# Kernel tuning notes

Measured on AMD Instinct MI355X. Metric: run time of the kernel, lower is better.

The kernel has to match this reference:

```python
import jax, jax.numpy as jnp
import numpy as np

# ---- model / data constants ----
B, N, D, L = 32, 96, 64, 5          # graphs, nodes per graph, hidden, layers
EP = 768                             # directed edges per graph (symmetrized in to_dense)
NODE_VOCAB = 11                      # matches LocalFWL2(..., 11, 5, 'instance')
EDGE_VOCAB = 5                       # edge labels 0..4; index 5 = 'no edge' embedding row
EPS = 1e-5


def setup_inputs() -> dict:
    key = jax.random.key(0)
    ks = jax.random.split(key, 12)
    # block-contiguous batch: graph b owns nodes [b*N, (b+1)*N)
    x = jax.random.randint(ks[0], (B * N,), 0, NODE_VOCAB)
    u = jax.random.randint(ks[1], (B, EP), 0, N)
    v = jax.random.randint(ks[2], (B, EP), 0, N)
    off = (jnp.arange(B) * N)[:, None]
    edge_index = jnp.stack([(u + off).reshape(-1), (v + off).reshape(-1)], axis=0)
    edge_attr = jax.random.randint(ks[3], (B * EP,), 0, EDGE_VOCAB)
    s = 0.1
    inv = 1.0 / np.sqrt(D)
    return {
        "x": x,
        "edge_index": edge_index,
        "edge_attr": edge_attr,
        "node_emb": jax.random.normal(ks[4], (NODE_VOCAB, D), jnp.float32) * s,
        "edge_emb": jax.random.normal(ks[5], (EDGE_VOCAB + 1, D), jnp.float32) * s,
        "W1": jax.random.normal(ks[6], (L, D, D), jnp.float32) * inv,
        "b1": jnp.zeros((L, D), jnp.float32),
        "W2": jax.random.normal(ks[7], (L, D, D), jnp.float32) * inv,
        "b2": jnp.zeros((L, D), jnp.float32),
        "Wm": jax.random.normal(ks[8], (L, D, D), jnp.float32) * inv,
        "bm": jnp.zeros((L, D), jnp.float32),
        "gamma": jnp.ones((L, D), jnp.float32),
        "beta": jnp.zeros((L, D), jnp.float32),
        "pool_w": jax.random.normal(ks[9], (D, 1), jnp.float32) * inv,
        "pool_b": jnp.zeros((1,), jnp.float32),
    }


def reference(x, edge_index, edge_attr, node_emb, edge_emb,
              W1, b1, W2, b2, Wm, bm, gamma, beta, pool_w, pool_b):
    # ---- to_dense: sparse edge list -> dense per-graph edge-label matrix ----
    g = edge_index[0] // N
    u = edge_index[0] % N
    v = edge_index[1] % N
    A = jnp.full((B, N, N), EDGE_VOCAB, dtype=jnp.int32)        # EDGE_VOCAB = no-edge
    ea = edge_attr.astype(jnp.int32)
    A = A.at[g, u, v].set(ea)
    A = A.at[g, v, u].set(ea)                                    # undirected
    adj = (A != EDGE_VOCAB).astype(node_emb.dtype)               # [B,N,N]

    # ---- pair-state init: W_uv = h_u + h_v + edge_emb(A_uv) ----
    H = node_emb[x.reshape(B, N)]                                # [B,N,D]
    W = H[:, :, None, :] + H[:, None, :, :] + edge_emb[A]        # [B,N,N,D]

    # ---- local FWL(2) layers ----
    for l in range(L):
        h1 = jax.nn.relu(jnp.einsum('buwd,de->buwe', W, W1[l]) + b1[l])
        h2 = jax.nn.relu(jnp.einsum('bwvd,de->bwve', W, W2[l]) + b2[l])
        # aggregate over w restricted to neighbors of v (local FWL2)
        M = jnp.einsum('buwd,bwv,bwvd->buvd', h1, adj, h2)       # [B,N,N,D]
        W = W + jnp.einsum('buvd,de->buve', M, Wm[l]) + bm[l]
        # instance norm over the pair dims (u,v), per graph, per channel
        mu = W.mean(axis=(1, 2), keepdims=True)
        var = W.var(axis=(1, 2), keepdims=True)
        W = gamma[l] * (W - mu) * jax.lax.rsqrt(var + EPS) + beta[l]
        W = jax.nn.relu(W)

    # ---- pooling: sum over all pairs, then Linear(D, 1), squeeze ----
    pooled = W.sum(axis=(1, 2))                                  # [B,D]
    return (pooled @ pool_w + pool_b).squeeze(-1)                # [B]
```

## Files before the change

kernel.cpp:

```cpp
#include <hip/hip_runtime.h>
#include <hip/hip_bf16.h>

#define B_ 32
#define N_ 96
#define D_ 64
#define L_ 5
#define BE_ 24576
#define NN_ 9216
#define BNN_ 294912
#define EPS_ 1e-5f
#define INV_NN (1.0f/9216.0f)

typedef unsigned short u16;
typedef unsigned int u32;
typedef __attribute__((ext_vector_type(8))) short bf16x8;
typedef __attribute__((ext_vector_type(4))) float f32x4;

__device__ __forceinline__ float bf2f(u16 r){ return __uint_as_float(((u32)r) << 16); }
__device__ __forceinline__ u32 f2bf(float f){
  u32 u = __float_as_uint(f);
  return (u + 0x7fffu + ((u >> 16) & 1u)) >> 16;
}
__device__ __forceinline__ u32 pack2(float lo, float hi){
  return f2bf(lo) | (f2bf(hi) << 16);
}

__global__ void k_scatter(const int* __restrict__ ei, const int* __restrict__ ea,
                          int* __restrict__ A)
{
  int e = blockIdx.x * 256 + threadIdx.x;
  if (e >= BE_) return;
  int a = ei[e], bnode = ei[BE_ + e];
  int g = a / N_;
  int u = a % N_;
  int v = bnode % N_;
  int lab = ea[e] & 7;
  int base = g * NN_;
  atomicMax(&A[base + u * N_ + v], ((e + 1) << 3) | lab);
  atomicMax(&A[base + v * N_ + u], ((BE_ + e + 1) << 3) | lab);
}

__launch_bounds__(256)
__global__ void k_winit(const int* __restrict__ x, const int* __restrict__ A,
                        const float* __restrict__ nemb, const float* __restrict__ eemb,
                        u16* __restrict__ W)
{
  int gid = blockIdx.x * 256 + threadIdx.x;
  int d = (gid & 15) * 4;
  int p = gid >> 4;
  int b = p / NN_;
  int rem = p % NN_;
  int u = rem / N_;
  int v = rem % N_;
  int xu = x[b * N_ + u], xv = x[b * N_ + v];
  int pk = A[p];
  int lab = pk ? (pk & 7) : 5;
  float4 nu = *(const float4*)(nemb + xu * 64 + d);
  float4 nv = *(const float4*)(nemb + xv * 64 + d);
  float4 ee = *(const float4*)(eemb + lab * 64 + d);
  uint2 o;
  o.x = pack2(nu.x + nv.x + ee.x, nu.y + nv.y + ee.y);
  o.y = pack2(nu.z + nv.z + ee.z, nu.w + nv.w + ee.w);
  ((uint2*)W)[gid] = o;
}

__global__ void k_prep(const float* __restrict__ W1, const float* __restrict__ W2,
                       const float* __restrict__ Wm, u16* __restrict__ WT)
{
  int idx = blockIdx.x * 256 + threadIdx.x;
  if (idx >= 15 * 4096) return;
  int l3 = idx >> 12;
  int r  = idx & 4095;
  int e = r >> 6, d = r & 63;
  int l = l3 / 3, which = l3 % 3;
  const float* s = which == 0 ? W1 : which == 1 ? W2 : Wm;
  WT[idx] = (u16)f2bf(s[l * 4096 + d * 64 + e]);
}

__launch_bounds__(128)
__global__ void k_ns(const float* __restrict__ pst, const float* __restrict__ gml,
                     const float* __restrict__ btl, float* __restrict__ nsF)
{
  __shared__ float nsS[128];
  const int b = blockIdx.x;
  const int tid = threadIdx.x;
  const float* p = pst + ((size_t)b * 144) * 128 + tid;
  float a0 = 0.f, a1 = 0.f, a2 = 0.f, a3 = 0.f;
  for (int i = 0; i < 144; i += 4) {
    a0 += p[(size_t)i * 128];
    a1 += p[(size_t)(i + 1) * 128];
    a2 += p[(size_t)(i + 2) * 128];
    a3 += p[(size_t)(i + 3) * 128];
  }
  nsS[tid] = (a0 + a1) + (a2 + a3);
  __syncthreads();
  if (tid < 64) {
    float S1 = nsS[tid], S2 = nsS[64 + tid];
    float mu = S1 * INV_NN;
    float var = fmaf(S2, INV_NN, -mu * mu);
    float s0 = gml[tid] * rsqrtf(var + EPS_);
    nsF[((size_t)b * 64 + tid) * 2]     = s0;
    nsF[((size_t)b * 64 + tid) * 2 + 1] = fmaf(-mu, s0, btl[tid]);
  }
}

__launch_bounds__(256, 8)
__global__ void k_lin2(const u16* __restrict__ W, const u16* __restrict__ WT1,
                       const u16* __restrict__ WT2,
                       const float* __restrict__ b1l, const float* __restrict__ b2l,
                       const int* __restrict__ A, const float* __restrict__ nsF,
                       int use_norm, u16* __restrict__ h1, u16* __restrict__ g2)
{
  __shared__ u16 Cs[64 * 136];
  const int tid = threadIdx.x;
  const int wave = tid >> 6, lane = tid & 63;
  const int lm = lane & 15, lg = lane >> 4;
  const int b = blockIdx.x / 72;
  const int qbase = (blockIdx.x % 72) * 128;

  float sc[2][8], sh[2][8];
  if (use_norm) {
    #pragma unroll
    for (int s = 0; s < 2; ++s) {
      int d0 = s * 32 + lg * 8;
      #pragma unroll
      for (int j = 0; j < 8; j += 2) {
        float4 t = *(const float4*)(nsF + ((size_t)b * 64 + d0 + j) * 2);
        sc[s][j] = t.x; sh[s][j] = t.y; sc[s][j + 1] = t.z; sh[s][j + 1] = t.w;
      }
    }
  } else {
    #pragma unroll
    for (int s = 0; s < 2; ++s)
      #pragma unroll
      for (int j = 0; j < 8; ++j) { sc[s][j] = 1.f; sh[s][j] = 0.f; }
  }

  bf16x8 bF[2][2];
  int flags[2];
  #pragma unroll
  for (int qt = 0; qt < 2; ++qt) {
    int q = qbase + wave * 32 + qt * 16 + lm;
    const u16* wrow = W + ((size_t)b * NN_ + q) * 64;
    flags[qt] = A[b * NN_ + q];
    #pragma unroll
    for (int s = 0; s < 2; ++s) {
      bf16x8 raw = *(const bf16x8*)(wrow + s * 32 + lg * 8);
      if (use_norm) {
        bf16x8 bb;
        #pragma unroll
        for (int j = 0; j < 8; ++j) {
          float v = bf2f((u16)raw[j]);
          v = fmaxf(fmaf(v, sc[s][j], sh[s][j]), 0.f);
          bb[j] = (short)f2bf(v);
        }
        bF[qt][s] = bb;
      } else {
        bF[qt][s] = raw;
      }
    }
  }

  const f32x4 zf = {0.f, 0.f, 0.f, 0.f};

  {
    bf16x8 aF[4][2];
    #pragma unroll
    for (int et = 0; et < 4; ++et)
      #pragma unroll
      for (int s = 0; s < 2; ++s)
        aF[et][s] = *(const bf16x8*)(WT1 + (et * 16 + lm) * 64 + s * 32 + lg * 8);
    float4 bsv[4];
    #pragma unroll
    for (int et = 0; et < 4; ++et) bsv[et] = *(const float4*)(b1l + et * 16 + lg * 4);
    #pragma unroll
    for (int qt = 0; qt < 2; ++qt) {
      f32x4 acc[4] = {zf, zf, zf, zf};
      #pragma unroll
      for (int s = 0; s < 2; ++s)
        #pragma unroll
        for (int et = 0; et < 4; ++et)
          acc[et] = __builtin_amdgcn_mfma_f32_16x16x32_bf16(aF[et][s], bF[qt][s], acc[et], 0, 0, 0);
      int col = wave * 32 + qt * 16 + lm;
      #pragma unroll
      for (int et = 0; et < 4; ++et) {
        float bv[4] = {bsv[et].x, bsv[et].y, bsv[et].z, bsv[et].w};
        #pragma unroll
        for (int r = 0; r < 4; ++r)
          Cs[(et * 16 + lg * 4 + r) * 136 + col] = (u16)f2bf(fmaxf(acc[et][r] + bv[r], 0.f));
      }
    }
  }
  __syncthreads();
  {
    u16* ob = h1 + (size_t)b * 64 * NN_ + qbase;
    for (int i = tid; i < 1024; i += 256) {
      int e = i >> 4, qc = (i & 15) * 8;
      uint4 val = *(const uint4*)&Cs[e * 136 + qc];
      *(uint4*)(ob + (size_t)e * NN_ + qc) = val;
    }
  }
  __syncthreads();

  {
    bf16x8 aF[4][2];
    #pragma unroll
    for (int et = 0; et < 4; ++et)
      #pragma unroll
      for (int s = 0; s < 2; ++s)
        aF[et][s] = *(const bf16x8*)(WT2 + (et * 16 + lm) * 64 + s * 32 + lg * 8);
    float4 bsv[4];
    #pragma unroll
    for (int et = 0; et < 4; ++et) bsv[et] = *(const float4*)(b2l + et * 16 + lg * 4);
    #pragma unroll
    for (int qt = 0; qt < 2; ++qt) {
      f32x4 acc[4] = {zf, zf, zf, zf};
      #pragma unroll
      for (int s = 0; s < 2; ++s)
        #pragma unroll
        for (int et = 0; et < 4; ++et)
          acc[et] = __builtin_amdgcn_mfma_f32_16x16x32_bf16(aF[et][s], bF[qt][s], acc[et], 0, 0, 0);
      int col = wave * 32 + qt * 16 + lm;
      #pragma unroll
      for (int et = 0; et < 4; ++et) {
        float bv[4] = {bsv[et].x, bsv[et].y, bsv[et].z, bsv[et].w};
        #pragma unroll
        for (int r = 0; r < 4; ++r) {
          float v = fmaxf(acc[et][r] + bv[r], 0.f);
          if (!flags[qt]) v = 0.f;
          Cs[(et * 16 + lg * 4 + r) * 136 + col] = (u16)f2bf(v);
        }
      }
    }
  }
  __syncthreads();
  {
    u16* ob = g2 + (size_t)b * 64 * NN_ + qbase;
    for (int i = tid; i < 1024; i += 256) {
      int e = i >> 4, qc = (i & 15) * 8;
      uint4 val = *(const uint4*)&Cs[e * 136 + qc];
      *(uint4*)(ob + (size_t)e * NN_ + qc) = val;
    }
  }
}

__launch_bounds__(256, 4)
__global__ void k_einsum(const u16* __restrict__ h1, const u16* __restrict__ g2n,
                         u16* __restrict__ M)
{
  __shared__ u32 Bt[96 * 60];
  u16* Cst = (u16*)Bt;
  const int tid = threadIdx.x;
  const int wave = tid >> 6, lane = tid & 63;
  const int lm = lane & 15, lg = lane >> 4;
  const int bd = blockIdx.x;
  const u16* h1p = h1 + (size_t)bd * NN_;
  const u16* g2p = g2n + (size_t)bd * NN_;
  const int u0 = (wave & 1) * 48, v0 = (wave >> 1) * 48;

  #pragma unroll
  for (int it = 0; it < 9; ++it) {
    int p = it * 256 + tid;
    int wp = p / 48, vh = (p % 48) * 2;
    u32 a = *(const u32*)(g2p + (2 * wp) * 96 + vh);
    u32 c = *(const u32*)(g2p + (2 * wp + 1) * 96 + vh);
    Bt[vh * 60 + wp]       = (a & 0xffffu) | (c << 16);
    Bt[(vh + 1) * 60 + wp] = (a >> 16) | (c & 0xffff0000u);
  }

  bf16x8 aF[3][3];
  #pragma unroll
  for (int t = 0; t < 3; ++t)
    #pragma unroll
    for (int s = 0; s < 3; ++s)
      aF[t][s] = *(const bf16x8*)(h1p + (u0 + t * 16 + lm) * 96 + s * 32 + lg * 8);
  __syncthreads();

  const f32x4 zf = {0.f, 0.f, 0.f, 0.f};
  f32x4 acc[3][3];
  #pragma unroll
  for (int i = 0; i < 3; ++i)
    #pragma unroll
    for (int j = 0; j < 3; ++j) acc[i][j] = zf;

  #pragma unroll
  for (int s = 0; s < 3; ++s) {
    bf16x8 bb[3];
    #pragma unroll
    for (int vt = 0; vt < 3; ++vt)
      bb[vt] = *(const bf16x8*)&Bt[(v0 + vt * 16 + lm) * 60 + s * 16 + lg * 4];
    #pragma unroll
    for (int ut = 0; ut < 3; ++ut)
      #pragma unroll
      for (int vt = 0; vt < 3; ++vt)
        acc[ut][vt] = __builtin_amdgcn_mfma_f32_16x16x32_bf16(aF[ut][s], bb[vt], acc[ut][vt], 0, 0, 0);
  }
  __syncthreads();

  #pragma unroll
  for (int ut = 0; ut < 3; ++ut)
    #pragma unroll
    for (int vt = 0; vt < 3; ++vt)
      #pragma unroll
      for (int r = 0; r < 4; ++r)
        Cst[(u0 + ut * 16 + lg * 4 + r) * 104 + v0 + vt * 16 + lm] = (u16)f2bf(acc[ut][vt][r]);
  __syncthreads();
  u16* Mp = M + (size_t)bd * NN_;
  for (int i = tid; i < 1152; i += 256) {
    int u = i / 12, vc = (i % 12) * 8;
    uint4 val = *(const uint4*)&Cst[u * 104 + vc];
    *(uint4*)(Mp + u * 96 + vc) = val;
  }
}

__launch_bounds__(128)
__global__ void k_update(const u16* __restrict__ M, const u16* __restrict__ WmT,
                         const float* __restrict__ bml, u16* __restrict__ W,
                         const float* __restrict__ nsF, int use_norm,
                         float* __restrict__ pst)
{
  __shared__ u16 Mt[64 * 64];
  __shared__ float red[2][128];
  const int tid = threadIdx.x;
  const int wave = tid >> 6, lane = tid & 63;
  const int lm = lane & 15, lg = lane >> 4;
  const int b = blockIdx.x / 144;
  const int qi = blockIdx.x % 144;
  const int qblk = qi * 64;

  bf16x8 aF[4][2];
  #pragma unroll
  for (int et = 0; et < 4; ++et)
    #pragma unroll
    for (int s = 0; s < 2; ++s)
      aF[et][s] = *(const bf16x8*)(WmT + (et * 16 + lm) * 64 + s * 32 + lg * 8);

  uint2 wres[2][4];
  #pragma unroll
  for (int qtL = 0; qtL < 2; ++qtL) {
    int qg = qblk + (wave * 2 + qtL) * 16 + lm;
    const u16* Wp = W + ((size_t)b * NN_ + qg) * 64;
    #pragma unroll
    for (int et = 0; et < 4; ++et)
      wres[qtL][et] = *(const uint2*)(Wp + et * 16 + lg * 4);
  }

  float scn[4][4], shn[4][4];
  if (use_norm) {
    #pragma unroll
    for (int et = 0; et < 4; ++et) {
      int e0 = et * 16 + lg * 4;
      float4 t0 = *(const float4*)(nsF + ((size_t)b * 64 + e0) * 2);
      float4 t1 = *(const float4*)(nsF + ((size_t)b * 64 + e0) * 2 + 4);
      scn[et][0] = t0.x; shn[et][0] = t0.y; scn[et][1] = t0.z; shn[et][1] = t0.w;
      scn[et][2] = t1.x; shn[et][2] = t1.y; scn[et][3] = t1.z; shn[et][3] = t1.w;
    }
  } else {
    #pragma unroll
    for (int et = 0; et < 4; ++et)
      #pragma unroll
      for (int r = 0; r < 4; ++r) { scn[et][r] = 1.f; shn[et][r] = 0.f; }
  }

  {
    const int dpl = tid >> 1;
    const int qob = tid & 1;
    const u16* Mb = M + (size_t)(b * 64 + dpl) * NN_ + qblk;
    #pragma unroll
    for (int t = 0; t < 4; ++t) {
      int qo = qob + t * 2;
      uint4 v = *(const uint4*)(Mb + qo * 8);
      u32 ws[4] = {v.x, v.y, v.z, v.w};
      #pragma unroll
      for (int h = 0; h < 4; ++h) {
        int j0 = h * 2;
        int q0 = qo * 8 + j0;
        int slot0 = (dpl >> 3) ^ j0 ^ (qo & 7);
        int slot1 = (dpl >> 3) ^ (j0 + 1) ^ (qo & 7);
        Mt[q0 * 64 + slot0 * 8 + (dpl & 7)]       = (u16)(ws[h] & 0xffffu);
        Mt[(q0 + 1) * 64 + slot1 * 8 + (dpl & 7)] = (u16)(ws[h] >> 16);
      }
    }
  }
  __syncthreads();

  const f32x4 zf = {0.f, 0.f, 0.f, 0.f};
  f32x4 acc[2][4];
  #pragma unroll
  for (int i = 0; i < 2; ++i)
    #pragma unroll
    for (int j = 0; j < 4; ++j) acc[i][j] = zf;

  #pragma unroll
  for (int qtL = 0; qtL < 2; ++qtL) {
    int ql = (wave * 2 + qtL) * 16 + lm;
    bf16x8 bF[2];
    #pragma unroll
    for (int s = 0; s < 2; ++s) {
      int slot = (s * 4 + lg) ^ (ql & 7) ^ ((ql >> 3) & 7);
      bF[s] = *(const bf16x8*)&Mt[ql * 64 + slot * 8];
    }
    #pragma unroll
    for (int s = 0; s < 2; ++s)
      #pragma unroll
      for (int et = 0; et < 4; ++et)
        acc[qtL][et] = __builtin_amdgcn_mfma_f32_16x16x32_bf16(aF[et][s], bF[s], acc[qtL][et], 0, 0, 0);
  }

  float s1[4][4], s2[4][4];
  #pragma unroll
  for (int i = 0; i < 4; ++i)
    #pragma unroll
    for (int j = 0; j < 4; ++j) { s1[i][j] = 0.f; s2[i][j] = 0.f; }

  #pragma unroll
  for (int et = 0; et < 4; ++et) {
    int e0 = et * 16 + lg * 4;
    float4 bs = *(const float4*)(bml + e0);
    float bv[4] = {bs.x, bs.y, bs.z, bs.w};
    #pragma unroll
    for (int qtL = 0; qtL < 2; ++qtL) {
      int qg = qblk + (wave * 2 + qtL) * 16 + lm;
      u16* Wp = W + ((size_t)b * NN_ + qg) * 64 + e0;
      uint2 wo = wres[qtL][et];
      float wv[4] = {bf2f((u16)(wo.x & 0xffff)), bf2f((u16)(wo.x >> 16)),
                     bf2f((u16)(wo.y & 0xffff)), bf2f((u16)(wo.y >> 16))};
      float o[4];
      #pragma unroll
      for (int r = 0; r < 4; ++r) {
        float res = use_norm ? fmaxf(fmaf(wv[r], scn[et][r], shn[et][r]), 0.f) : wv[r];
        float val = acc[qtL][et][r] + bv[r] + res;
        o[r] = val;
        s1[et][r] += val;
        s2[et][r] = fmaf(val, val, s2[et][r]);
      }
      uint2 ov;
      ov.x = pack2(o[0], o[1]);
      ov.y = pack2(o[2], o[3]);
      *(uint2*)Wp = ov;
    }
  }

  #pragma unroll
  for (int et = 0; et < 4; ++et)
    #pragma unroll
    for (int r = 0; r < 4; ++r) {
      float a = s1[et][r], c = s2[et][r];
      a += __shfl_xor(a, 1, 64); a += __shfl_xor(a, 2, 64);
      a += __shfl_xor(a, 4, 64); a += __shfl_xor(a, 8, 64);
      c += __shfl_xor(c, 1, 64); c += __shfl_xor(c, 2, 64);
      c += __shfl_xor(c, 4, 64); c += __shfl_xor(c, 8, 64);
      if (lm == 0) {
        int e = et * 16 + lg * 4 + r;
        red[wave][e]      = a;
        red[wave][64 + e] = c;
      }
    }
  __syncthreads();
  if (tid < 128)
    pst[((size_t)b * 144 + qi) * 128 + tid] = red[0][tid] + red[1][tid];
}

__launch_bounds__(256)
__global__ void k_pool(const u16* __restrict__ W,
                       const float* __restrict__ nsF,
                       const float* __restrict__ pw, const float* __restrict__ pb,
                       float* __restrict__ out)
{
  const int b = blockIdx.x / 24;
  const int chunk = blockIdx.x % 24;
  const int tid = threadIdx.x;
  const int e = tid & 63;
  float scl = nsF[((size_t)b * 64 + e) * 2];
  float shf = nsF[((size_t)b * 64 + e) * 2 + 1];
  float pwv = pw[e];
  const u16* base = W + (size_t)b * NN_ * 64 + chunk * 24576;
  float s = 0.f;
  for (int k = 0; k < 96; k++) {
    float w = bf2f(base[k * 256 + tid]);
    s += fmaxf(fmaf(w, scl, shf), 0.f) * pwv;
  }
  for (int o = 32; o; o >>= 1) s += __shfl_down(s, o, 64);
  __shared__ float rs[4];
  if ((tid & 63) == 0) rs[tid >> 6] = s;
  __syncthreads();
  if (tid == 0) {
    float t = rs[0] + rs[1] + rs[2] + rs[3];
    if (chunk == 0) t += pb[0];
    atomicAdd(&out[b], t);
  }
}

extern "C" void kernel_launch(void* const* d_in, const int* in_sizes, int n_in,
                              void* d_out, int out_size, void* d_ws, size_t ws_size,
                              hipStream_t stream) {
  const int*   x    = (const int*)d_in[0];
  const int*   ei   = (const int*)d_in[1];
  const int*   ea   = (const int*)d_in[2];
  const float* nemb = (const float*)d_in[3];
  const float* eemb = (const float*)d_in[4];
  const float* W1   = (const float*)d_in[5];
  const float* b1   = (const float*)d_in[6];
  const float* W2   = (const float*)d_in[7];
  const float* b2   = (const float*)d_in[8];
  const float* Wm   = (const float*)d_in[9];
  const float* bm   = (const float*)d_in[10];
  const float* gm   = (const float*)d_in[11];
  const float* bt   = (const float*)d_in[12];
  const float* pw   = (const float*)d_in[13];
  const float* pb   = (const float*)d_in[14];

  char* ws = (char*)d_ws;
  const size_t OFF_A  = 0;
  const size_t OFF_W  = 1179648;
  const size_t OFF_H1 = 38928384;
  const size_t OFF_G2 = 76677120;
  const size_t OFF_M  = 114425856;
  const size_t OFF_PS = 152174592;
  const size_t OFF_NF = 154533888;
  const size_t OFF_WT = 154550272;
  const size_t NEED   = OFF_WT + 122880;
  if (ws_size < NEED) return;

  int*   A     = (int*)(ws + OFF_A);
  u16*   W     = (u16*)(ws + OFF_W);
  u16*   h1    = (u16*)(ws + OFF_H1);
  u16*   g2n   = (u16*)(ws + OFF_G2);
  u16*   M     = (u16*)(ws + OFF_M);
  float* pst   = (float*)(ws + OFF_PS);
  float* nsF   = (float*)(ws + OFF_NF);
  u16*   WT    = (u16*)(ws + OFF_WT);
  float* out   = (float*)d_out;

  hipMemsetAsync(A, 0, 1179648, stream);
  hipMemsetAsync(out, 0, 32 * sizeof(float), stream);

  k_prep<<<240, 256, 0, stream>>>(W1, W2, Wm, WT);
  k_scatter<<<96, 256, 0, stream>>>(ei, ea, A);
  k_winit<<<18432, 256, 0, stream>>>(x, A, nemb, eemb, W);

  for (int l = 0; l < L_; l++) {
    int un = (l > 0);
    if (un)
      k_ns<<<32, 128, 0, stream>>>(pst, gm + (l - 1) * 64, bt + (l - 1) * 64, nsF);
    k_lin2<<<2304, 256, 0, stream>>>(W, WT + (l * 3 + 0) * 4096, WT + (l * 3 + 1) * 4096,
                                     b1 + l * 64, b2 + l * 64, A, nsF, un, h1, g2n);
    k_einsum<<<2048, 256, 0, stream>>>(h1, g2n, M);
    k_update<<<4608, 128, 0, stream>>>(M, WT + (l * 3 + 2) * 4096, bm + l * 64, W,
                                       nsF, un, pst);
  }
  k_ns<<<32, 128, 0, stream>>>(pst, gm + 4 * 64, bt + 4 * 64, nsF);
  k_pool<<<768, 256, 0, stream>>>(W, nsF, pw, pb, out);
}
```

Measured before the change: 633.4 us.

## Fuse instance-norm stats finalize into consumers via atomic per-graph sums

Removes the separate k_ns kernel launches by having k_update atomically accumulate per-graph channel sums and sums of squares into a per-layer stats buffer. Consumer kernels (k_lin2, k_update, k_pool) then compute mean, variance, scale and shift on the fly from those sums. This saves five small launches and their serialization gaps. In exchange it adds float atomics, which make the sums nondeterministic, plus redundant rsqrt work in every block. It also drops the occupancy hint on k_lin2.

Result: no change. 621.7 us (-1.8%).

```diff
diff --git a/kernel.cpp b/kernel.cpp
--- a/kernel.cpp
+++ b/kernel.cpp
@@ -77,56 +77,42 @@
   WT[idx] = (u16)f2bf(s[l * 4096 + d * 64 + e]);
 }
 
-__launch_bounds__(128)
-__global__ void k_ns(const float* __restrict__ pst, const float* __restrict__ gml,
-                     const float* __restrict__ btl, float* __restrict__ nsF)
-{
-  __shared__ float nsS[128];
-  const int b = blockIdx.x;
-  const int tid = threadIdx.x;
-  const float* p = pst + ((size_t)b * 144) * 128 + tid;
-  float a0 = 0.f, a1 = 0.f, a2 = 0.f, a3 = 0.f;
-  for (int i = 0; i < 144; i += 4) {
-    a0 += p[(size_t)i * 128];
-    a1 += p[(size_t)(i + 1) * 128];
-    a2 += p[(size_t)(i + 2) * 128];
-    a3 += p[(size_t)(i + 3) * 128];
-  }
-  nsS[tid] = (a0 + a1) + (a2 + a3);
-  __syncthreads();
-  if (tid < 64) {
-    float S1 = nsS[tid], S2 = nsS[64 + tid];
-    float mu = S1 * INV_NN;
-    float var = fmaf(S2, INV_NN, -mu * mu);
-    float s0 = gml[tid] * rsqrtf(var + EPS_);
-    nsF[((size_t)b * 64 + tid) * 2]     = s0;
-    nsF[((size_t)b * 64 + tid) * 2 + 1] = fmaf(-mu, s0, btl[tid]);
-  }
-}
-
-__launch_bounds__(256, 8)
+__launch_bounds__(256)
 __global__ void k_lin2(const u16* __restrict__ W, const u16* __restrict__ WT1,
                        const u16* __restrict__ WT2,
                        const float* __restrict__ b1l, const float* __restrict__ b2l,
-                       const int* __restrict__ A, const float* __restrict__ nsF,
+                       const int* __restrict__ A,
+                       const float* __restrict__ stp, const float* __restrict__ gml,
+                       const float* __restrict__ btl,
                        int use_norm, u16* __restrict__ h1, u16* __restrict__ g2)
 {
   __shared__ u16 Cs[64 * 136];
+  __shared__ float nsS[128];
   const int tid = threadIdx.x;
   const int wave = tid >> 6, lane = tid & 63;
   const int lm = lane & 15, lg = lane >> 4;
   const int b = blockIdx.x / 72;
   const int qbase = (blockIdx.x % 72) * 128;
 
+  if (use_norm) {
+    if (tid < 128) nsS[tid] = stp[(size_t)b * 128 + tid];
+    __syncthreads();
+  }
+
   float sc[2][8], sh[2][8];
   if (use_norm) {
     #pragma unroll
     for (int s = 0; s < 2; ++s) {
       int d0 = s * 32 + lg * 8;
       #pragma unroll
-      for (int j = 0; j < 8; j += 2) {
-        float4 t = *(const float4*)(nsF + ((size_t)b * 64 + d0 + j) * 2);
-        sc[s][j] = t.x; sh[s][j] = t.y; sc[s][j + 1] = t.z; sh[s][j + 1] = t.w;
+      for (int j = 0; j < 8; ++j) {
+        int d = d0 + j;
+        float S1 = nsS[d], S2 = nsS[64 + d];
+        float mu = S1 * INV_NN;
+        float var = fmaf(S2, INV_NN, -mu * mu);
+        float s0 = gml[d] * rsqrtf(var + EPS_);
+        sc[s][j] = s0;
+        sh[s][j] = fmaf(-mu, s0, btl[d]);
       }
     }
   } else {
@@ -316,11 +302,13 @@
 __launch_bounds__(128)
 __global__ void k_update(const u16* __restrict__ M, const u16* __restrict__ WmT,
                          const float* __restrict__ bml, u16* __restrict__ W,
-                         const float* __restrict__ nsF, int use_norm,
-                         float* __restrict__ pst)
+                         const float* __restrict__ stp, const float* __restrict__ gml,
+                         const float* __restrict__ btl, int use_norm,
+                         float* __restrict__ sto)
 {
   __shared__ u16 Mt[64 * 64];
   __shared__ float red[2][128];
+  __shared__ float nsS[128];
   const int tid = threadIdx.x;
   const int wave = tid >> 6, lane = tid & 63;
   const int lm = lane & 15, lg = lane >> 4;
@@ -328,6 +316,10 @@
   const int qi = blockIdx.x % 144;
   const int qblk = qi * 64;
 
+  if (use_norm) {
+    if (tid < 128) nsS[tid] = stp[(size_t)b * 128 + tid];
+  }
+
   bf16x8 aF[4][2];
   #pragma unroll
   for (int et = 0; et < 4; ++et)
@@ -343,23 +335,6 @@
     #pragma unroll
     for (int et = 0; et < 4; ++et)
       wres[qtL][et] = *(const uint2*)(Wp + et * 16 + lg * 4);
-  }
-
-  float scn[4][4], shn[4][4];
-  if (use_norm) {
-    #pragma unroll
-    for (int et = 0; et < 4; ++et) {
-      int e0 = et * 16 + lg * 4;
-      float4 t0 = *(const float4*)(nsF + ((size_t)b * 64 + e0) * 2);
-      float4 t1 = *(const float4*)(nsF + ((size_t)b * 64 + e0) * 2 + 4);
-      scn[et][0] = t0.x; shn[et][0] = t0.y; scn[et][1] = t0.z; shn[et][1] = t0.w;
-      scn[et][2] = t1.x; shn[et][2] = t1.y; scn[et][3] = t1.z; shn[et][3] = t1.w;
-    }
-  } else {
-    #pragma unroll
-    for (int et = 0; et < 4; ++et)
-      #pragma unroll
-      for (int r = 0; r < 4; ++r) { scn[et][r] = 1.f; shn[et][r] = 0.f; }
   }
 
   {
@@ -383,6 +358,29 @@
     }
   }
   __syncthreads();
+
+  float scn[4][4], shn[4][4];
+  if (use_norm) {
+    #pragma unroll
+    for (int et = 0; et < 4; ++et) {
+      int e0 = et * 16 + lg * 4;
+      #pragma unroll
+      for (int r = 0; r < 4; ++r) {
+        int e = e0 + r;
+        float S1 = nsS[e], S2 = nsS[64 + e];
+        float mu = S1 * INV_NN;
+        float var = fmaf(S2, INV_NN, -mu * mu);
+        float s0 = gml[e] * rsqrtf(var + EPS_);
+        scn[et][r] = s0;
+        shn[et][r] = fmaf(-mu, s0, btl[e]);
+      }
+    }
+  } else {
+    #pragma unroll
+    for (int et = 0; et < 4; ++et)
+      #pragma unroll
+      for (int r = 0; r < 4; ++r) { scn[et][r] = 1.f; shn[et][r] = 0.f; }
+  }
 
   const f32x4 zf = {0.f, 0.f, 0.f, 0.f};
   f32x4 acc[2][4];
@@ -458,21 +456,29 @@
     }
   __syncthreads();
   if (tid < 128)
-    pst[((size_t)b * 144 + qi) * 128 + tid] = red[0][tid] + red[1][tid];
+    atomicAdd(&sto[(size_t)b * 128 + tid], red[0][tid] + red[1][tid]);
 }
 
 __launch_bounds__(256)
 __global__ void k_pool(const u16* __restrict__ W,
-                       const float* __restrict__ nsF,
+                       const float* __restrict__ stp,
+                       const float* __restrict__ gml, const float* __restrict__ btl,
                        const float* __restrict__ pw, const float* __restrict__ pb,
                        float* __restrict__ out)
 {
+  __shared__ float nsS[128];
   const int b = blockIdx.x / 24;
   const int chunk = blockIdx.x % 24;
   const int tid = threadIdx.x;
+  if (tid < 128) nsS[tid] = stp[(size_t)b * 128 + tid];
+  __syncthreads();
   const int e = tid & 63;
-  float scl = nsF[((size_t)b * 64 + e) * 2];
-  float shf = nsF[((size_t)b * 64 + e) * 2 + 1];
+  float S1 = nsS[e], S2 = nsS[64 + e];
+  float mu = S1 * INV_NN;
+  float var = fmaf(S2, INV_NN, -mu * mu);
+  float rsig = rsqrtf(var + EPS_);
+  float scl = gml[e] * rsig;
+  float shf = fmaf(-mu, scl, btl[e]);
   float pwv = pw[e];
   const u16* base = W + (size_t)b * NN_ * 64 + chunk * 24576;
   float s = 0.f;
@@ -516,9 +522,8 @@
   const size_t OFF_H1 = 38928384;
   const size_t OFF_G2 = 76677120;
   const size_t OFF_M  = 114425856;
-  const size_t OFF_PS = 152174592;
-  const size_t OFF_NF = 154533888;
-  const size_t OFF_WT = 154550272;
+  const size_t OFF_ST = 152174592;
+  const size_t OFF_WT = 152256512;
   const size_t NEED   = OFF_WT + 122880;
   if (ws_size < NEED) return;
 
@@ -527,12 +532,12 @@
   u16*   h1    = (u16*)(ws + OFF_H1);
   u16*   g2n   = (u16*)(ws + OFF_G2);
   u16*   M     = (u16*)(ws + OFF_M);
-  float* pst   = (float*)(ws + OFF_PS);
-  float* nsF   = (float*)(ws + OFF_NF);
+  float* stats = (float*)(ws + OFF_ST);
   u16*   WT    = (u16*)(ws + OFF_WT);
   float* out   = (float*)d_out;
 
   hipMemsetAsync(A, 0, 1179648, stream);
+  hipMemsetAsync(stats, 0, 81920, stream);
   hipMemsetAsync(out, 0, 32 * sizeof(float), stream);
 
   k_prep<<<240, 256, 0, stream>>>(W1, W2, Wm, WT);
@@ -541,14 +546,17 @@
 
   for (int l = 0; l < L_; l++) {
     int un = (l > 0);
-    if (un)
-      k_ns<<<32, 128, 0, stream>>>(pst, gm + (l - 1) * 64, bt + (l - 1) * 64, nsF);
+    const float* stp = un ? stats + (size_t)(l - 1) * 4096 : stats;
+    const float* gml = un ? gm + (l - 1) * 64 : gm;
+    const float* btl = un ? bt + (l - 1) * 64 : bt;
+    float* sto = stats + (size_t)l * 4096;
     k_lin2<<<2304, 256, 0, stream>>>(W, WT + (l * 3 + 0) * 4096, WT + (l * 3 + 1) * 4096,
-                                     b1 + l * 64, b2 + l * 64, A, nsF, un, h1, g2n);
+                                     b1 + l * 64, b2 + l * 64, A, stp, gml, btl,
+                                     un, h1, g2n);
     k_einsum<<<2048, 256, 0, stream>>>(h1, g2n, M);
     k_update<<<4608, 128, 0, stream>>>(M, WT + (l * 3 + 2) * 4096, bm + l * 64, W,
-                                       nsF, un, pst);
-  }
-  k_ns<<<32, 128, 0, stream>>>(pst, gm + 4 * 64, bt + 4 * 64, nsF);
-  k_pool<<<768, 256, 0, stream>>>(W, nsF, pw, pb, out);
-}
+                                       stp, gml, btl, un, sto);
+  }
+  k_pool<<<768, 256, 0, stream>>>(W, stats + 4 * 4096, gm + 4 * 64, bt + 4 * 64,
+                                  pw, pb, out);
+}
```
